# Optimization experiments

Hardware: AMD Instinct MI355X
Metric: run time of the kernel (lower is better)

The kernel has to match this reference:

```python
import jax, jax.numpy as jnp
import numpy as np

TEMPERATURE = 0.5
EPS = 1e-12  # torch F.normalize eps


def setup_inputs() -> dict:
    key = jax.random.key(0)
    k1, k2 = jax.random.split(key)
    z_i = jax.random.normal(k1, (32, 128, 128), dtype=jnp.float32)
    z_j = jax.random.normal(k2, (32, 128, 128), dtype=jnp.float32)
    return {"z_i": z_i, "z_j": z_j}


def _l2_normalize(x):
    # matches torch F.normalize(dim=1): x / max(||x||, eps)
    n = jnp.sqrt(jnp.sum(x * x, axis=1, keepdims=True))
    return x / jnp.maximum(n, EPS)


def _off_diagonal(a):
    # rows of a with the diagonal removed, row-major order -> [n, n-1]
    n = a.shape[0]
    return a.reshape(-1)[:-1].reshape(n - 1, n + 1)[:, 1:].reshape(n, n - 1)


def reference(z_i, z_j):
    B, S, D = z_i.shape
    N = B * S
    zi = _l2_normalize(z_i.reshape(N, D))
    zj = _l2_normalize(z_j.reshape(N, D))
    r = jnp.concatenate([zi, zj], axis=0)              # [2N, D]
    sim = r @ r.T                                      # [2N, 2N]
    # positives: off-diagonals at +/-N (unaffected by the diag -inf fill)
    pos = jnp.concatenate([jnp.diagonal(sim, N), jnp.diagonal(sim, -N)])  # [2N]
    # negatives: all non-diagonal entries, row-major (== torch boolean-mask view)
    neg = _off_diagonal(sim)                           # [2N, 2N-1]
    logits = jnp.concatenate([pos[:, None], neg], axis=1) / TEMPERATURE  # [2N, 2N]
    # labels are all 0 -> CE(sum) / 2N == mean of -log_softmax[:, 0]
    loss = -jax.nn.log_softmax(logits, axis=1)[:, 0]
    return jnp.sum(loss) / (2 * N)
```

## Files before the change

### kernel.cpp

```cpp
#include <hip/hip_runtime.h>
#include <hip/hip_bf16.h>
#include <math.h>

#define NPAIR 4096
#define D 128
#define TWO_N 8192
#define NSLAB 32
#define ALPHA 1.6986436f

typedef short bf16x8 __attribute__((ext_vector_type(8)));
typedef float f32x4 __attribute__((ext_vector_type(4)));

__device__ __forceinline__ void async_ld16(void* lds, const void* g) {
    __builtin_amdgcn_global_load_lds(
        (__attribute__((address_space(1))) const unsigned int*)g,
        (__attribute__((address_space(3))) unsigned int*)lds, 16, 0, 0);
}

__device__ inline unsigned short f2bf(float x) {
    union { float f; unsigned u; } v; v.f = x;
    unsigned u = v.u;
    unsigned r = u + 0x7fffu + ((u >> 16) & 1u);
    return (unsigned short)(r >> 16);
}

__global__ __launch_bounds__(256) void norm_kernel(const float* __restrict__ zi,
                                                   const float* __restrict__ zj,
                                                   unsigned int* __restrict__ Rb,
                                                   float* __restrict__ pos,
                                                   float* __restrict__ out) {
    if (blockIdx.x == 0 && threadIdx.x == 0) out[0] = 0.f;
    int k = blockIdx.x * 4 + (threadIdx.x >> 6);
    int t = threadIdx.x & 63;
    const float2 a = *(const float2*)(zi + k * D + 2 * t);
    const float2 b = *(const float2*)(zj + k * D + 2 * t);
    float si = a.x * a.x + a.y * a.y;
    float sj = b.x * b.x + b.y * b.y;
    float dt = a.x * b.x + a.y * b.y;
    #pragma unroll
    for (int m = 1; m < 64; m <<= 1) {
        si += __shfl_xor(si, m, 64);
        sj += __shfl_xor(sj, m, 64);
        dt += __shfl_xor(dt, m, 64);
    }
    float ii = 1.0f / fmaxf(sqrtf(si), 1e-12f);
    float ij = 1.0f / fmaxf(sqrtf(sj), 1e-12f);
    if (t == 0) pos[k] = dt * ii * ij;
    ii *= ALPHA; ij *= ALPHA;
    unsigned short b0 = f2bf(a.x * ii), b1 = f2bf(a.y * ii);
    Rb[k * (D / 2) + t] = (unsigned)b0 | ((unsigned)b1 << 16);
    b0 = f2bf(b.x * ij); b1 = f2bf(b.y * ij);
    Rb[(k + NPAIR) * (D / 2) + t] = (unsigned)b0 | ((unsigned)b1 << 16);
}

__global__ __launch_bounds__(256, 3) void simexp_kernel(const uint4* __restrict__ Rb,
                                                        float* __restrict__ rspart) {
    __shared__ uint4 Bs[4][3][256];
    const int bi = blockIdx.x >> 3;
    const int jc = blockIdx.x & 7;
    const int tid = threadIdx.x;
    const int wave = tid >> 6, lane = tid & 63;
    const int rp = lane & 15, q = lane >> 4;

    bf16x8 afr[4][4];
    {
        const uint4* Ab = Rb + (bi * 64 + rp) * 16;
        #pragma unroll
        for (int kt = 0; kt < 4; ++kt)
            #pragma unroll
            for (int rt = 0; rt < 4; ++rt)
                afr[kt][rt] = *(const bf16x8*)&Ab[rt * 256 + kt * 4 + q];
    }

    const char* Rbb = (const char*)Rb;
    const char* gpanel = Rbb + (size_t)(jc * 1024 + wave * 16) * 256;
    char* lpanel = (char*)&Bs[wave][0][0];

    float rs[16];
    #pragma unroll
    for (int i = 0; i < 16; ++i) rs[i] = 0.f;

    #pragma unroll
    for (int j = 0; j < 2; ++j)
        #pragma unroll
        for (int it = 0; it < 4; ++it) {
            int cr = it * 4 + q;
            async_ld16(lpanel + j * 4096 + it * 1024,
                       gpanel + (j * 64 + cr) * 256 + ((rp ^ cr) << 4));
        }

    const int diagbase = bi * 64 - jc * 1024;

    #pragma unroll
    for (int jt = 0; jt < 16; ++jt) {
        if (jt < 14) __builtin_amdgcn_s_waitcnt(0x0F74);
        else         __builtin_amdgcn_s_waitcnt(0x0F70);

        const int cur = jt % 3;
        bf16x8 bfr[4];
        #pragma unroll
        for (int kt = 0; kt < 4; ++kt)
            bfr[kt] = *(const bf16x8*)&Bs[wave][cur][rp * 16 + ((kt * 4 + q) ^ rp)];

        if (jt < 14) {
            const int nb = (jt + 2) % 3;
            #pragma unroll
            for (int it = 0; it < 4; ++it) {
                int cr = it * 4 + q;
                async_ld16(lpanel + nb * 4096 + it * 1024,
                           gpanel + ((jt + 2) * 64 + cr) * 256 + ((rp ^ cr) << 4));
            }
        }

        f32x4 acc[4] = {};
        #pragma unroll
        for (int kt = 0; kt < 4; ++kt)
            #pragma unroll
            for (int rt = 0; rt < 4; ++rt)
                acc[rt] = __builtin_amdgcn_mfma_f32_16x16x32_bf16(
                    afr[kt][rt], bfr[kt], acc[rt], 0, 0, 0);

        if (jt * 64 == diagbase) {
            #pragma unroll
            for (int rt = 0; rt < 4; ++rt)
                #pragma unroll
                for (int r = 0; r < 4; ++r) {
                    int ro = rt * 16 + q * 4 + r;
                    int co = wave * 16 + rp;
                    float e = __builtin_amdgcn_exp2f(acc[rt][r]);
                    rs[rt * 4 + r] += (ro == co) ? 0.f : e;
                }
        } else {
            #pragma unroll
            for (int rt = 0; rt < 4; ++rt)
                #pragma unroll
                for (int r = 0; r < 4; ++r)
                    rs[rt * 4 + r] += __builtin_amdgcn_exp2f(acc[rt][r]);
        }
    }

    #pragma unroll
    for (int i = 0; i < 16; ++i) {
        float v = rs[i];
        v += __shfl_xor(v, 1, 64);
        v += __shfl_xor(v, 2, 64);
        v += __shfl_xor(v, 4, 64);
        v += __shfl_xor(v, 8, 64);
        rs[i] = v;
    }
    if (rp == 0) {
        const int slab = jc * 4 + wave;
        const int rowb = bi * 64 + q * 4;
        #pragma unroll
        for (int rt = 0; rt < 4; ++rt)
            #pragma unroll
            for (int r = 0; r < 4; ++r)
                rspart[slab * TWO_N + rowb + rt * 16 + r] = rs[rt * 4 + r];
    }
}

__global__ __launch_bounds__(256) void finalize_kernel(const float* __restrict__ rspart,
                                                       const float* __restrict__ pos,
                                                       float* __restrict__ out) {
    __shared__ float red[4];
    int tid = threadIdx.x;
    float local = 0.f;
    #pragma unroll
    for (int i = 0; i < 2; ++i) {
        int k = blockIdx.x * 512 + i * 256 + tid;
        float rsum = 0.f;
        #pragma unroll
        for (int p = 0; p < NSLAB; ++p) rsum += rspart[p * TWO_N + k];
        float ps = pos[k & (NPAIR - 1)];
        float p2 = ps + ps;
        local += logf(rsum + __expf(p2)) - p2;
    }
    #pragma unroll
    for (int m = 1; m < 64; m <<= 1) local += __shfl_xor(local, m, 64);
    if ((tid & 63) == 0) red[tid >> 6] = local;
    __syncthreads();
    if (tid == 0) {
        float s = red[0] + red[1] + red[2] + red[3];
        atomicAdd(out, s * (1.0f / (float)TWO_N));
    }
}

extern "C" void kernel_launch(void* const* d_in, const int* in_sizes, int n_in,
                              void* d_out, int out_size, void* d_ws, size_t ws_size,
                              hipStream_t stream) {
    const float* zi = (const float*)d_in[0];
    const float* zj = (const float*)d_in[1];
    char* ws = (char*)d_ws;
    unsigned int* Rb = (unsigned int*)ws;
    float* rspart = (float*)(ws + 2 * 1024 * 1024);
    float* pos = (float*)(ws + 3 * 1024 * 1024);

    norm_kernel<<<NPAIR / 4, 256, 0, stream>>>(zi, zj, Rb, pos, (float*)d_out);
    simexp_kernel<<<128 * 8, 256, 0, stream>>>((const uint4*)Rb, rspart);
    finalize_kernel<<<16, 256, 0, stream>>>(rspart, pos, (float*)d_out);
}
```

Baseline: 85.10 us.

## Switch similarity GEMM operands from bf16 to fp8 MFMA with repacked layout

The normalized embeddings are now stored as packed fp8 in a permuted byte layout instead of bf16, and the similarity matmul uses fp8 16x16x32 MFMA. This halves the operand bytes moved through global memory and LDS, halves the LDS staging buffers, and raises the occupancy hint from 3 to 4 blocks. The cost is much lower precision in the similarity logits before they are exponentiated, which risks larger error in the loss.

```diff
diff --git a/kernel.cpp b/kernel.cpp
--- a/kernel.cpp
+++ b/kernel.cpp
@@ -8,8 +8,8 @@
 #define NSLAB 32
 #define ALPHA 1.6986436f
 
-typedef short bf16x8 __attribute__((ext_vector_type(8)));
 typedef float f32x4 __attribute__((ext_vector_type(4)));
+typedef long lx2 __attribute__((ext_vector_type(2)));
 
 __device__ __forceinline__ void async_ld16(void* lds, const void* g) {
     __builtin_amdgcn_global_load_lds(
@@ -17,16 +17,9 @@
         (__attribute__((address_space(3))) unsigned int*)lds, 16, 0, 0);
 }
 
-__device__ inline unsigned short f2bf(float x) {
-    union { float f; unsigned u; } v; v.f = x;
-    unsigned u = v.u;
-    unsigned r = u + 0x7fffu + ((u >> 16) & 1u);
-    return (unsigned short)(r >> 16);
-}
-
 __global__ __launch_bounds__(256) void norm_kernel(const float* __restrict__ zi,
                                                    const float* __restrict__ zj,
-                                                   unsigned int* __restrict__ Rb,
+                                                   unsigned char* __restrict__ Rb,
                                                    float* __restrict__ pos,
                                                    float* __restrict__ out) {
     if (blockIdx.x == 0 && threadIdx.x == 0) out[0] = 0.f;
@@ -47,34 +40,38 @@
     float ij = 1.0f / fmaxf(sqrtf(sj), 1e-12f);
     if (t == 0) pos[k] = dt * ii * ij;
     ii *= ALPHA; ij *= ALPHA;
-    unsigned short b0 = f2bf(a.x * ii), b1 = f2bf(a.y * ii);
-    Rb[k * (D / 2) + t] = (unsigned)b0 | ((unsigned)b1 << 16);
-    b0 = f2bf(b.x * ij); b1 = f2bf(b.y * ij);
-    Rb[(k + NPAIR) * (D / 2) + t] = (unsigned)b0 | ((unsigned)b1 << 16);
+    int c = t >> 2;
+    int posb = (c & 3) * 32 + (c >> 2) * 8 + 2 * (t & 3);
+    int r0 = __builtin_amdgcn_cvt_pk_fp8_f32(a.x * ii, a.y * ii, 0, false);
+    *(unsigned short*)(Rb + (size_t)k * 128 + posb) = (unsigned short)r0;
+    int r1 = __builtin_amdgcn_cvt_pk_fp8_f32(b.x * ij, b.y * ij, 0, false);
+    *(unsigned short*)(Rb + (size_t)(k + NPAIR) * 128 + posb) = (unsigned short)r1;
 }
 
-__global__ __launch_bounds__(256, 3) void simexp_kernel(const uint4* __restrict__ Rb,
+__global__ __launch_bounds__(256, 4) void simexp_kernel(const unsigned char* __restrict__ Rb,
                                                         float* __restrict__ rspart) {
-    __shared__ uint4 Bs[4][3][256];
+    __shared__ uint4 Bs[4][3][128];
     const int bi = blockIdx.x >> 3;
     const int jc = blockIdx.x & 7;
     const int tid = threadIdx.x;
     const int wave = tid >> 6, lane = tid & 63;
     const int rp = lane & 15, q = lane >> 4;
 
-    bf16x8 afr[4][4];
+    long afr[4][4];
     {
-        const uint4* Ab = Rb + (bi * 64 + rp) * 16;
+        const unsigned char* Ab = Rb + (size_t)(bi * 64 + rp) * 128 + q * 32;
         #pragma unroll
-        for (int kt = 0; kt < 4; ++kt)
-            #pragma unroll
-            for (int rt = 0; rt < 4; ++rt)
-                afr[kt][rt] = *(const bf16x8*)&Ab[rt * 256 + kt * 4 + q];
+        for (int rt = 0; rt < 4; ++rt) {
+            lx2 h0 = *(const lx2*)(Ab + rt * 16 * 128);
+            lx2 h1 = *(const lx2*)(Ab + rt * 16 * 128 + 16);
+            afr[0][rt] = h0.x;  afr[1][rt] = h0.y;
+            afr[2][rt] = h1.x;  afr[3][rt] = h1.y;
+        }
     }
 
-    const char* Rbb = (const char*)Rb;
-    const char* gpanel = Rbb + (size_t)(jc * 1024 + wave * 16) * 256;
+    const unsigned char* gslab = Rb + (size_t)(jc * 1024 + wave * 16) * 128;
     char* lpanel = (char*)&Bs[wave][0][0];
+    const int laneoff = (lane >> 3) * 128 + (((lane & 7) ^ ((lane >> 3) & 7)) << 4);
 
     float rs[16];
     #pragma unroll
@@ -83,42 +80,40 @@
     #pragma unroll
     for (int j = 0; j < 2; ++j)
         #pragma unroll
-        for (int it = 0; it < 4; ++it) {
-            int cr = it * 4 + q;
-            async_ld16(lpanel + j * 4096 + it * 1024,
-                       gpanel + (j * 64 + cr) * 256 + ((rp ^ cr) << 4));
-        }
+        for (int d = 0; d < 2; ++d)
+            async_ld16(lpanel + j * 2048 + d * 1024,
+                       gslab + j * 8192 + d * 1024 + laneoff);
 
     const int diagbase = bi * 64 - jc * 1024;
+    const int slot0 = rp * 8;
+    const int sw = rp & 7;
 
     #pragma unroll
     for (int jt = 0; jt < 16; ++jt) {
-        if (jt < 14) __builtin_amdgcn_s_waitcnt(0x0F74);
+        if (jt < 14) __builtin_amdgcn_s_waitcnt(0x0F72);
         else         __builtin_amdgcn_s_waitcnt(0x0F70);
 
         const int cur = jt % 3;
-        bf16x8 bfr[4];
-        #pragma unroll
-        for (int kt = 0; kt < 4; ++kt)
-            bfr[kt] = *(const bf16x8*)&Bs[wave][cur][rp * 16 + ((kt * 4 + q) ^ rp)];
+        const uint4* P = &Bs[wave][cur][0];
+        lx2 v0 = *(const lx2*)&P[slot0 + ((q * 2 + 0) ^ sw)];
+        lx2 v1 = *(const lx2*)&P[slot0 + ((q * 2 + 1) ^ sw)];
 
         if (jt < 14) {
             const int nb = (jt + 2) % 3;
             #pragma unroll
-            for (int it = 0; it < 4; ++it) {
-                int cr = it * 4 + q;
-                async_ld16(lpanel + nb * 4096 + it * 1024,
-                           gpanel + ((jt + 2) * 64 + cr) * 256 + ((rp ^ cr) << 4));
-            }
+            for (int d = 0; d < 2; ++d)
+                async_ld16(lpanel + nb * 2048 + d * 1024,
+                           gslab + (jt + 2) * 8192 + d * 1024 + laneoff);
         }
 
         f32x4 acc[4] = {};
         #pragma unroll
-        for (int kt = 0; kt < 4; ++kt)
-            #pragma unroll
-            for (int rt = 0; rt < 4; ++rt)
-                acc[rt] = __builtin_amdgcn_mfma_f32_16x16x32_bf16(
-                    afr[kt][rt], bfr[kt], acc[rt], 0, 0, 0);
+        for (int rt = 0; rt < 4; ++rt) {
+            acc[rt] = __builtin_amdgcn_mfma_f32_16x16x32_fp8_fp8(afr[0][rt], v0.x, acc[rt], 0, 0, 0);
+            acc[rt] = __builtin_amdgcn_mfma_f32_16x16x32_fp8_fp8(afr[1][rt], v0.y, acc[rt], 0, 0, 0);
+            acc[rt] = __builtin_amdgcn_mfma_f32_16x16x32_fp8_fp8(afr[2][rt], v1.x, acc[rt], 0, 0, 0);
+            acc[rt] = __builtin_amdgcn_mfma_f32_16x16x32_fp8_fp8(afr[3][rt], v1.y, acc[rt], 0, 0, 0);
+        }
 
         if (jt * 64 == diagbase) {
             #pragma unroll
@@ -191,11 +186,11 @@
     const float* zi = (const float*)d_in[0];
     const float* zj = (const float*)d_in[1];
     char* ws = (char*)d_ws;
-    unsigned int* Rb = (unsigned int*)ws;
-    float* rspart = (float*)(ws + 2 * 1024 * 1024);
-    float* pos = (float*)(ws + 3 * 1024 * 1024);
+    unsigned char* Rb = (unsigned char*)ws;
+    float* rspart = (float*)(ws + 1 * 1024 * 1024);
+    float* pos = (float*)(ws + 2 * 1024 * 1024);
 
     norm_kernel<<<NPAIR / 4, 256, 0, stream>>>(zi, zj, Rb, pos, (float*)d_out);
-    simexp_kernel<<<128 * 8, 256, 0, stream>>>((const uint4*)Rb, rspart);
+    simexp_kernel<<<128 * 8, 256, 0, stream>>>(Rb, rspart);
     finalize_kernel<<<16, 256, 0, stream>>>(rspart, pos, (float*)d_out);
 }
```

New measurement: 78.96 us. -7.2%, faster.
